# Kernel tuning notes

Hardware: AMD Instinct MI355X
Metric: run time of the kernel (lower is better)

## Reference

```python
import jax, jax.numpy as jnp
import numpy as np

B, D, H, W, Q = 16, 768, 64, 64, 128


def setup_inputs() -> dict:
    key = jax.random.key(0)
    ks = jax.random.split(key, 6)
    s = 0.02  # param init scale
    return {
        "visual_feat": jax.random.normal(ks[0], (B, D, H, W), jnp.float32),
        "text_feat": jax.random.normal(ks[1], (B, Q, D), jnp.float32),
        "Wq": jax.random.normal(ks[2], (D, D), jnp.float32) * s,
        "bq": jnp.zeros((D,), jnp.float32),
        "Wk": jax.random.normal(ks[3], (D, D), jnp.float32) * s,
        "bk": jnp.zeros((D,), jnp.float32),
        "Wv": jax.random.normal(ks[4], (D, D), jnp.float32) * s,
        "bv": jnp.zeros((D,), jnp.float32),
    }


def _entropy_weights(x):
    # x: [B, T, D] -> softmax over features, per-token entropy, softmax over tokens -> [B, T]
    p = jax.nn.softmax(x, axis=-1)
    ent = -jnp.sum(p * jnp.log(p + 1e-9), axis=-1)
    return jax.nn.softmax(ent, axis=-1)


def reference(visual_feat, text_feat, Wq, bq, Wk, bk, Wv, bv):
    b, d, h, w = visual_feat.shape
    vf = visual_feat.reshape(b, d, h * w).transpose(0, 2, 1)  # [B, N, D]
    ve = _entropy_weights(vf)          # [B, N]
    te = _entropy_weights(text_feat)   # [B, Q]
    q = vf @ Wq.T + bq                 # [B, N, D]
    k = text_feat @ Wk.T + bk          # [B, Q, D]
    v = text_feat @ Wv.T + bv          # [B, Q, D]
    attn = jnp.einsum('bnd,bqd->bnq', q, k) / jnp.sqrt(jnp.float32(d))
    attn = attn * (ve[:, :, None] * te[:, None, :])  # entropy outer-product modulation
    attn = jax.nn.softmax(attn, axis=-1)
    enhanced = jnp.einsum('bnq,bqd->bnd', attn, v)   # [B, N, D]
    return enhanced.transpose(0, 2, 1).reshape(b, d, h, w)
```

## Files before the change

kernel.cpp:

```cpp
#include <hip/hip_runtime.h>

#define B_ 16
#define D_ 768
#define N_ 4096
#define Q_ 128

typedef __attribute__((ext_vector_type(4))) float f32x4;
typedef __attribute__((ext_vector_type(8))) short short8;
typedef __attribute__((ext_vector_type(4))) short sv4;

__device__ __forceinline__ unsigned short f2bf(float f) {
  union { float f; unsigned u; } x; x.f = f;
  unsigned u = x.u;
  unsigned r = u + 0x7fffu + ((u >> 16) & 1u);
  return (unsigned short)(r >> 16);
}
__device__ __forceinline__ float bf2f(unsigned short h) {
  union { unsigned u; float f; } x; x.u = ((unsigned)h) << 16;
  return x.f;
}

__global__ __launch_bounds__(256) void prep_kernel(
    const float* __restrict__ Wk, const float* __restrict__ Wv,
    const float* __restrict__ Wq,
    unsigned short* __restrict__ Wkb, unsigned short* __restrict__ Wvb,
    unsigned short* __restrict__ WqTb) {
  __shared__ float tile[32][33];
  const int z = blockIdx.z;
  const int t = threadIdx.x;
  if (z <= 1) {
    const float* src = z ? Wv : Wk;
    unsigned short* dst = z ? Wvb : Wkb;
    int i = (blockIdx.y * 24 + blockIdx.x) * 256 + t;
    float4 v = ((const float4*)src)[i];
    ushort4 o;
    o.x = f2bf(v.x); o.y = f2bf(v.y); o.z = f2bf(v.z); o.w = f2bf(v.w);
    ((ushort4*)dst)[i] = o;
  } else {
    int bx = blockIdx.x * 32, by = blockIdx.y * 32;
    int tx = t & 31, ty = t >> 5;
    #pragma unroll
    for (int i = 0; i < 32; i += 8)
      tile[ty + i][tx] = Wq[(size_t)(by + ty + i) * D_ + bx + tx];
    __syncthreads();
    #pragma unroll
    for (int i = 0; i < 32; i += 8)
      WqTb[(size_t)(bx + ty + i) * D_ + by + tx] = f2bf(tile[tx][ty + i]);
  }
}

__global__ __launch_bounds__(256) void text_prep_kernel(
    const float* __restrict__ text, unsigned short* __restrict__ textb,
    float* __restrict__ ent_t) {
  int row = blockIdx.x * 4 + (threadIdx.x >> 6);
  int lane = threadIdx.x & 63;
  const float4* src = (const float4*)(text + (size_t)row * D_);
  ushort4* dst = (ushort4*)(textb + (size_t)row * D_);
  float s = 0.f, tt = 0.f;
  #pragma unroll
  for (int j = 0; j < 3; j++) {
    float4 v = src[lane + 64 * j];
    float e0 = __expf(v.x), e1 = __expf(v.y), e2 = __expf(v.z), e3 = __expf(v.w);
    s += (e0 + e1) + (e2 + e3);
    tt += v.x * e0 + v.y * e1;
    tt += v.z * e2 + v.w * e3;
    ushort4 o;
    o.x = f2bf(v.x); o.y = f2bf(v.y); o.z = f2bf(v.z); o.w = f2bf(v.w);
    dst[lane + 64 * j] = o;
  }
  #pragma unroll
  for (int off = 32; off; off >>= 1) {
    s += __shfl_xor(s, off);
    tt += __shfl_xor(tt, off);
  }
  if (lane == 0) ent_t[row] = __logf(s) - tt / s;
}

__global__ __launch_bounds__(1024) void softmax_fused_kernel(
    const float* __restrict__ ent_v, float* __restrict__ vew,
    const float* __restrict__ ent_t, float* __restrict__ tew) {
  __shared__ float red[32];
  __shared__ float sv[128];
  const int b = blockIdx.x, t = threadIdx.x;
  if (b < 16) {
    const float* e = ent_v + (size_t)b * N_;
    float v[4];
    float m = -__builtin_inff();
    #pragma unroll
    for (int i = 0; i < 4; i++) { v[i] = e[t + 1024 * i]; m = fmaxf(m, v[i]); }
    #pragma unroll
    for (int off = 32; off; off >>= 1) m = fmaxf(m, __shfl_xor(m, off));
    int wv = t >> 6;
    if ((t & 63) == 0) red[wv] = m;
    __syncthreads();
    if (t < 16) {
      float x = red[t];
      #pragma unroll
      for (int off = 8; off; off >>= 1) x = fmaxf(x, __shfl_xor(x, off));
      red[t] = x;
    }
    __syncthreads();
    m = red[0];
    float ev[4];
    float s = 0.f;
    #pragma unroll
    for (int i = 0; i < 4; i++) { ev[i] = __expf(v[i] - m); s += ev[i]; }
    #pragma unroll
    for (int off = 32; off; off >>= 1) s += __shfl_xor(s, off);
    __syncthreads();
    if ((t & 63) == 0) red[wv] = s;
    __syncthreads();
    if (t < 16) {
      float x = red[t];
      #pragma unroll
      for (int off = 8; off; off >>= 1) x += __shfl_xor(x, off);
      red[t] = x;
    }
    __syncthreads();
    s = red[0];
    #pragma unroll
    for (int i = 0; i < 4; i++) vew[(size_t)b * N_ + t + 1024 * i] = ev[i] / s;
  } else {
    const int bb = b - 16;
    float v = 0.f;
    if (t < 128) { v = ent_t[bb * 128 + t]; sv[t] = v; }
    __syncthreads();
    if (t < 64) {
      float m = fmaxf(sv[t], sv[t + 64]);
      #pragma unroll
      for (int off = 32; off; off >>= 1) m = fmaxf(m, __shfl_xor(m, off));
      if (t == 0) red[0] = m;
    }
    __syncthreads();
    const float m = red[0];
    float e = 0.f;
    if (t < 128) { e = __expf(v - m); sv[t] = e; }
    __syncthreads();
    if (t < 64) {
      float s = sv[t] + sv[t + 64];
      #pragma unroll
      for (int off = 32; off; off >>= 1) s += __shfl_xor(s, off);
      if (t == 0) red[1] = s;
    }
    __syncthreads();
    if (t < 128) tew[bb * 128 + t] = e / red[1];
  }
}

__global__ __launch_bounds__(256) void gemm_kvT_kernel(
    const unsigned short* __restrict__ A, const unsigned short* __restrict__ Wkb,
    const float* __restrict__ bk, unsigned short* __restrict__ kb,
    const unsigned short* __restrict__ Wvb, const float* __restrict__ bv,
    unsigned short* __restrict__ vTb) {
  constexpr int LDA = 72;
  __shared__ unsigned short As[64 * LDA];
  __shared__ unsigned short Bs[64 * LDA];
  const bool isV = blockIdx.y >= 12;
  const unsigned short* Bm = isV ? Wvb : Wkb;
  const float* bias = isV ? bv : bk;
  unsigned short* C = isV ? vTb : kb;
  int m0 = blockIdx.x * 64, n0 = (isV ? blockIdx.y - 12 : blockIdx.y) * 64;
  int t = threadIdx.x, wave = t >> 6, lane = t & 63;
  int wm = (wave & 1) * 32, wn = (wave >> 1) * 32;
  int fl = lane & 15, fq = lane >> 4;
  f32x4 acc[2][2];
  #pragma unroll
  for (int i = 0; i < 2; i++)
    #pragma unroll
    for (int j = 0; j < 2; j++) acc[i][j] = {0.f, 0.f, 0.f, 0.f};
  for (int k0 = 0; k0 < D_; k0 += 64) {
    __syncthreads();
    #pragma unroll
    for (int i = 0; i < 2; i++) {
      int c = t + 256 * i;
      int sr = c >> 3, sc = (c & 7) * 8;
      *(uint4*)(As + sr * LDA + sc) = *(const uint4*)(A + (size_t)(m0 + sr) * D_ + k0 + sc);
      *(uint4*)(Bs + sr * LDA + sc) = *(const uint4*)(Bm + (size_t)(n0 + sr) * D_ + k0 + sc);
    }
    __syncthreads();
    #pragma unroll
    for (int ks = 0; ks < 2; ks++) {
      short8 afr[2], bfr[2];
      #pragma unroll
      for (int i = 0; i < 2; i++)
        afr[i] = *(const short8*)(As + (wm + i * 16 + fl) * LDA + ks * 32 + fq * 8);
      #pragma unroll
      for (int j = 0; j < 2; j++)
        bfr[j] = *(const short8*)(Bs + (wn + j * 16 + fl) * LDA + ks * 32 + fq * 8);
      #pragma unroll
      for (int i = 0; i < 2; i++)
        #pragma unroll
        for (int j = 0; j < 2; j++)
          acc[i][j] = __builtin_amdgcn_mfma_f32_16x16x32_bf16(afr[i], bfr[j], acc[i][j], 0, 0, 0);
    }
  }
  #pragma unroll
  for (int i = 0; i < 2; i++)
    #pragma unroll
    for (int j = 0; j < 2; j++) {
      int n = n0 + wn + j * 16 + fl;
      float bb = bias[n];
      #pragma unroll
      for (int r = 0; r < 4; r++) {
        int m = m0 + wm + i * 16 + fq * 4 + r;
        float val = acc[i][j][r] + bb;
        if (isV) {
          int bt = m >> 7, q = m & 127;
          C[((size_t)bt * D_ + n) * Q_ + q] = f2bf(val);
        } else {
          C[(size_t)m * D_ + n] = f2bf(val);
        }
      }
    }
}

__global__ __launch_bounds__(256) void gemm_kq_bias_kernel(
    const unsigned short* __restrict__ kb, const unsigned short* __restrict__ WqTb,
    unsigned short* __restrict__ kqb, const float* __restrict__ bq,
    float* __restrict__ skq) {
  constexpr int LDA = 72;
  __shared__ unsigned short As[64 * LDA];
  __shared__ unsigned short Bs[64 * LDA];
  const int t = threadIdx.x;
  if (blockIdx.y >= 12) {
    int idx = (blockIdx.y - 12) * 32 + blockIdx.x;
    int row = idx * 4 + (t >> 6);
    int lane = t & 63;
    const unsigned short* kr = kb + (size_t)row * D_;
    float s = 0.f;
    for (int k = lane; k < D_; k += 64) s += bq[k] * bf2f(kr[k]);
    #pragma unroll
    for (int off = 32; off; off >>= 1) s += __shfl_xor(s, off);
    if (lane == 0) skq[row] = s;
    return;
  }
  int m0 = blockIdx.x * 64, n0 = blockIdx.y * 64;
  int wave = t >> 6, lane = t & 63;
  int wm = (wave & 1) * 32, wn = (wave >> 1) * 32;
  int fl = lane & 15, fq = lane >> 4;
  f32x4 acc[2][2];
  #pragma unroll
  for (int i = 0; i < 2; i++)
    #pragma unroll
    for (int j = 0; j < 2; j++) acc[i][j] = {0.f, 0.f, 0.f, 0.f};
  for (int k0 = 0; k0 < D_; k0 += 64) {
    __syncthreads();
    #pragma unroll
    for (int i = 0; i < 2; i++) {
      int c = t + 256 * i;
      int sr = c >> 3, sc = (c & 7) * 8;
      *(uint4*)(As + sr * LDA + sc) = *(const uint4*)(kb + (size_t)(m0 + sr) * D_ + k0 + sc);
      *(uint4*)(Bs + sr * LDA + sc) = *(const uint4*)(WqTb + (size_t)(n0 + sr) * D_ + k0 + sc);
    }
    __syncthreads();
    #pragma unroll
    for (int ks = 0; ks < 2; ks++) {
      short8 afr[2], bfr[2];
      #pragma unroll
      for (int i = 0; i < 2; i++)
        afr[i] = *(const short8*)(As + (wm + i * 16 + fl) * LDA + ks * 32 + fq * 8);
      #pragma unroll
      for (int j = 0; j < 2; j++)
        bfr[j] = *(const short8*)(Bs + (wn + j * 16 + fl) * LDA + ks * 32 + fq * 8);
      #pragma unroll
      for (int i = 0; i < 2; i++)
        #pragma unroll
        for (int j = 0; j < 2; j++)
          acc[i][j] = __builtin_amdgcn_mfma_f32_16x16x32_bf16(afr[i], bfr[j], acc[i][j], 0, 0, 0);
    }
  }
  #pragma unroll
  for (int i = 0; i < 2; i++)
    #pragma unroll
    for (int j = 0; j < 2; j++) {
      int n = n0 + wn + j * 16 + fl;
      #pragma unroll
      for (int r = 0; r < 4; r++) {
        int m = m0 + wm + i * 16 + fq * 4 + r;
        kqb[(size_t)m * D_ + n] = f2bf(acc[i][j][r]);
      }
    }
}

__global__ __launch_bounds__(256, 2) void attn_s_kernel(
    const float* __restrict__ vis,
    const unsigned short* __restrict__ kq,
    float* __restrict__ S,
    float* __restrict__ ent_v)
{
  constexpr int LA = 68;
  constexpr int LB = 72;
  __shared__ unsigned short As[64 * LA];
  __shared__ unsigned short Bs[128 * LB];
  __shared__ float esh[512];

  const int bb = blockIdx.x >> 6;
  const int n0 = (blockIdx.x & 63) * 64;
  const int t = threadIdx.x;
  const int wave = t >> 6, lane = t & 63;
  const int fl = lane & 15, fq = lane >> 4;
  const int wm = (wave & 1) * 32;
  const int wq = (wave >> 1) * 64;

  const float* abase = vis + (size_t)bb * D_ * N_ + n0;
  const unsigned short* bbase = kq + (size_t)bb * Q_ * D_;

  f32x4 acc[2][4];
  #pragma unroll
  for (int i = 0; i < 2; i++)
    #pragma unroll
    for (int j = 0; j < 4; j++) acc[i][j] = {0.f, 0.f, 0.f, 0.f};

  const int smi = t & 63;
  const int ph = t >> 6;
  float es = 0.f, ets = 0.f;

  for (int k0 = 0; k0 < D_; k0 += 64) {
    __syncthreads();
    #pragma unroll
    for (int i = 0; i < 8; i++) {
      const int kk = 2 * (ph + 4 * i);
      const float v0 = abase[(size_t)(k0 + kk) * N_ + smi];
      const float v1 = abase[(size_t)(k0 + kk + 1) * N_ + smi];
      const float e0 = __expf(v0), e1 = __expf(v1);
      es += e0 + e1;
      ets += v0 * e0 + v1 * e1;
      const unsigned pk = (unsigned)f2bf(v0) | ((unsigned)f2bf(v1) << 16);
      *(unsigned*)(As + smi * LA + kk) = pk;
    }
    #pragma unroll
    for (int i = 0; i < 4; i++) {
      const int c = t + 256 * i;
      const int q = c >> 3, kc = (c & 7) * 8;
      const uint4 v = *(const uint4*)(bbase + (size_t)q * D_ + k0 + kc);
      *(uint4*)(Bs + q * LB + kc) = v;
    }
    __syncthreads();
    #pragma unroll
    for (int ks = 0; ks < 2; ks++) {
      short8 afr[2], bfr[4];
      #pragma unroll
      for (int i = 0; i < 2; i++) {
        const unsigned short* pa = As + (wm + i * 16 + fl) * LA + ks * 32 + fq * 8;
        sv4 lo = *(const sv4*)pa;
        sv4 hi = *(const sv4*)(pa + 4);
        afr[i] = __builtin_shufflevector(lo, hi, 0, 1, 2, 3, 4, 5, 6, 7);
      }
      #pragma unroll
      for (int j = 0; j < 4; j++)
        bfr[j] = *(const short8*)(Bs + (wq + j * 16 + fl) * LB + ks * 32 + fq * 8);
      #pragma unroll
      for (int i = 0; i < 2; i++)
        #pragma unroll
        for (int j = 0; j < 4; j++)
          acc[i][j] = __builtin_amdgcn_mfma_f32_16x16x32_bf16(afr[i], bfr[j], acc[i][j], 0, 0, 0);
    }
  }

  esh[t] = es;
  esh[256 + t] = ets;
  __syncthreads();
  if (t < 64) {
    const float Sx = esh[t] + esh[t + 64] + esh[t + 128] + esh[t + 192];
    const float Tx = esh[256 + t] + esh[320 + t] + esh[384 + t] + esh[448 + t];
    ent_v[(size_t)bb * N_ + n0 + t] = __logf(Sx) - Tx / Sx;
  }

  float* sbase = S + ((size_t)bb * N_ + n0) * Q_;
  #pragma unroll
  for (int i = 0; i < 2; i++)
    #pragma unroll
    for (int j = 0; j < 4; j++)
      #pragma unroll
      for (int r = 0; r < 4; r++)
        sbase[(size_t)(wm + i * 16 + fq * 4 + r) * Q_ + wq + j * 16 + fl] = acc[i][j][r];
}

__global__ __launch_bounds__(256, 2) void attn_pv_kernel(
    const float* __restrict__ S,
    const unsigned short* __restrict__ vT,
    const float* __restrict__ ve,
    const float* __restrict__ te,
    const float* __restrict__ skq,
    float* __restrict__ out)
{
  constexpr int LP = 136;
  __shared__ unsigned short Ps[64 * LP];
  __shared__ unsigned short Vs[64 * LP];
  __shared__ float stats[2][64][2];

  const int bb = blockIdx.x >> 6;
  const int n0 = (blockIdx.x & 63) * 64;
  const int t = threadIdx.x;
  const int wave = t >> 6, lane = t & 63;
  const int fl = lane & 15, fq = lane >> 4;
  const int wm = (wave & 1) * 32;
  const int wq = (wave >> 1) * 64;

  f32x4 acc[2][4];
  const float* sbase = S + ((size_t)bb * N_ + n0) * Q_;
  #pragma unroll
  for (int i = 0; i < 2; i++)
    #pragma unroll
    for (int j = 0; j < 4; j++)
      #pragma unroll
      for (int r = 0; r < 4; r++)
        acc[i][j][r] = sbase[(size_t)(wm + i * 16 + fq * 4 + r) * Q_ + wq + j * 16 + fl];

  const float rsD = 0.03608439182435161f;
  float tev[4], skv[4];
  #pragma unroll
  for (int j = 0; j < 4; j++) {
    int q = wq + j * 16 + fl;
    tev[j] = te[bb * Q_ + q];
    skv[j] = skq[bb * Q_ + q];
  }
  float vev4[2][4];
  #pragma unroll
  for (int i = 0; i < 2; i++)
    #pragma unroll
    for (int r = 0; r < 4; r++)
      vev4[i][r] = ve[(size_t)bb * N_ + n0 + wm + i * 16 + fq * 4 + r];

  float rmax[2][4], rsum[2][4];
  #pragma unroll
  for (int i = 0; i < 2; i++)
    #pragma unroll
    for (int r = 0; r < 4; r++) rmax[i][r] = -__builtin_inff();
  #pragma unroll
  for (int i = 0; i < 2; i++)
    #pragma unroll
    for (int j = 0; j < 4; j++)
      #pragma unroll
      for (int r = 0; r < 4; r++) {
        float L = (acc[i][j][r] + skv[j]) * rsD * vev4[i][r] * tev[j];
        acc[i][j][r] = L;
        rmax[i][r] = fmaxf(rmax[i][r], L);
      }
  #pragma unroll
  for (int off = 1; off < 16; off <<= 1)
    #pragma unroll
    for (int i = 0; i < 2; i++)
      #pragma unroll
      for (int r = 0; r < 4; r++)
        rmax[i][r] = fmaxf(rmax[i][r], __shfl_xor(rmax[i][r], off));
  #pragma unroll
  for (int i = 0; i < 2; i++)
    #pragma unroll
    for (int r = 0; r < 4; r++) rsum[i][r] = 0.f;
  #pragma unroll
  for (int i = 0; i < 2; i++)
    #pragma unroll
    for (int j = 0; j < 4; j++)
      #pragma unroll
      for (int r = 0; r < 4; r++) {
        float e = __expf(acc[i][j][r] - rmax[i][r]);
        acc[i][j][r] = e;
        rsum[i][r] += e;
      }
  #pragma unroll
  for (int off = 1; off < 16; off <<= 1)
    #pragma unroll
    for (int i = 0; i < 2; i++)
      #pragma unroll
      for (int r = 0; r < 4; r++) rsum[i][r] += __shfl_xor(rsum[i][r], off);

  const int qh = wq >> 6;
  if (fl == 0) {
    #pragma unroll
    for (int i = 0; i < 2; i++)
      #pragma unroll
      for (int r = 0; r < 4; r++) {
        int m = wm + i * 16 + fq * 4 + r;
        stats[qh][m][0] = rmax[i][r];
        stats[qh][m][1] = rsum[i][r];
      }
  }
  __syncthreads();
  float fac[2][4];
  #pragma unroll
  for (int i = 0; i < 2; i++)
    #pragma unroll
    for (int r = 0; r < 4; r++) {
      int m = wm + i * 16 + fq * 4 + r;
      float M2 = stats[1 - qh][m][0], S2 = stats[1 - qh][m][1];
      float Mf = fmaxf(rmax[i][r], M2);
      float sf = rsum[i][r] * __expf(rmax[i][r] - Mf) + S2 * __expf(M2 - Mf);
      fac[i][r] = __expf(rmax[i][r] - Mf) / sf;
    }
  #pragma unroll
  for (int i = 0; i < 2; i++)
    #pragma unroll
    for (int j = 0; j < 4; j++)
      #pragma unroll
      for (int r = 0; r < 4; r++) {
        int m = wm + i * 16 + fq * 4 + r;
        int q = wq + j * 16 + fl;
        Ps[m * LP + q] = f2bf(acc[i][j][r] * fac[i][r]);
      }

  const int wd = (wave & 1) * 32;
  const int wm2 = (wave >> 1) * 32;
  for (int dc = 0; dc < 12; dc++) {
    __syncthreads();
    const unsigned short* vbase = vT + ((size_t)bb * D_ + dc * 64) * Q_;
    #pragma unroll
    for (int i = 0; i < 4; i++) {
      const int c = t + 256 * i;
      const int d = c >> 4, qc = (c & 15) * 8;
      *(uint4*)(Vs + d * LP + qc) = *(const uint4*)(vbase + (size_t)d * Q_ + qc);
    }
    __syncthreads();
    f32x4 acc2[2][2];
    #pragma unroll
    for (int i = 0; i < 2; i++)
      #pragma unroll
      for (int j = 0; j < 2; j++) acc2[i][j] = {0.f, 0.f, 0.f, 0.f};
    #pragma unroll
    for (int ks = 0; ks < 4; ks++) {
      short8 vfr[2], pfr[2];
      #pragma unroll
      for (int i = 0; i < 2; i++)
        vfr[i] = *(const short8*)(Vs + (wd + i * 16 + fl) * LP + ks * 32 + fq * 8);
      #pragma unroll
      for (int j = 0; j < 2; j++)
        pfr[j] = *(const short8*)(Ps + (wm2 + j * 16 + fl) * LP + ks * 32 + fq * 8);
      #pragma unroll
      for (int i = 0; i < 2; i++)
        #pragma unroll
        for (int j = 0; j < 2; j++)
          acc2[i][j] = __builtin_amdgcn_mfma_f32_16x16x32_bf16(vfr[i], pfr[j], acc2[i][j], 0, 0, 0);
    }
    float* obase = out + ((size_t)bb * D_ + dc * 64) * N_ + n0;
    #pragma unroll
    for (int i = 0; i < 2; i++)
      #pragma unroll
      for (int j = 0; j < 2; j++) {
        int mm = wm2 + j * 16 + fl;
        #pragma unroll
        for (int r = 0; r < 4; r++) {
          int d = wd + i * 16 + fq * 4 + r;
          obase[(size_t)d * N_ + mm] = acc2[i][j][r];
        }
      }
  }
}

extern "C" void kernel_launch(void* const* d_in, const int* in_sizes, int n_in,
                              void* d_out, int out_size, void* d_ws, size_t ws_size,
                              hipStream_t stream) {
  const float* vis  = (const float*)d_in[0];
  const float* text = (const float*)d_in[1];
  const float* Wq   = (const float*)d_in[2];
  const float* bq   = (const float*)d_in[3];
  const float* Wk   = (const float*)d_in[4];
  const float* bk   = (const float*)d_in[5];
  const float* Wv   = (const float*)d_in[6];
  const float* bv   = (const float*)d_in[7];
  float* out = (float*)d_out;
  char* ws = (char*)d_ws;

  unsigned short* textb = (unsigned short*)(ws + 0);
  unsigned short* Wkb   = (unsigned short*)(ws + 3145728);
  unsigned short* Wvb   = (unsigned short*)(ws + 4325376);
  unsigned short* WqTb  = (unsigned short*)(ws + 5505024);
  unsigned short* kb    = (unsigned short*)(ws + 6684672);
  unsigned short* kqb   = (unsigned short*)(ws + 9830400);
  unsigned short* vTb   = (unsigned short*)(ws + 12976128);
  float* ent_t = (float*)(ws + 16121856);
  float* tew   = (float*)(ws + 16130048);
  float* ent_v = (float*)(ws + 16138240);
  float* vew   = (float*)(ws + 16400384);
  float* skq   = (float*)(ws + 16662528);
  float* Sbuf  = (float*)(ws + 16777216);

  prep_kernel<<<dim3(24, 24, 3), 256, 0, stream>>>(Wk, Wv, Wq, Wkb, Wvb, WqTb);
  text_prep_kernel<<<512, 256, 0, stream>>>(text, textb, ent_t);
  gemm_kvT_kernel<<<dim3(32, 24), 256, 0, stream>>>(textb, Wkb, bk, kb, Wvb, bv, vTb);
  gemm_kq_bias_kernel<<<dim3(32, 28), 256, 0, stream>>>(kb, WqTb, kqb, bq, skq);
  attn_s_kernel<<<1024, 256, 0, stream>>>(vis, kqb, Sbuf, ent_v);
  softmax_fused_kernel<<<32, 1024, 0, stream>>>(ent_v, vew, ent_t, tew);
  attn_pv_kernel<<<1024, 256, 0, stream>>>(Sbuf, vTb, vew, tew, skq, out);
}
```

Baseline: 436.6 us.

## Fuse score, softmax and PV stages into one cooperative attention kernel

Adds a single attention kernel that computes the QK scores and the visual entropy. It then does a grid-wide sync so the per-batch entropy normaliser can be summed with atomics, applies the entropy modulation and softmax in registers, and multiplies by V. This avoids writing and re-reading the fp32 score buffer and drops two kernel launches. It needs all 1024 blocks to be co-resident through a cooperative launch, and falls back to the old three-kernel path if occupancy is too low or the launch fails. The Z accumulator is zeroed in the prep kernel.

```diff
diff --git a/kernel.cpp b/kernel.cpp
--- a/kernel.cpp
+++ b/kernel.cpp
@@ -1,4 +1,5 @@
 #include <hip/hip_runtime.h>
+#include <hip/hip_cooperative_groups.h>
 
 #define B_ 16
 #define D_ 768
@@ -24,7 +25,7 @@
     const float* __restrict__ Wk, const float* __restrict__ Wv,
     const float* __restrict__ Wq,
     unsigned short* __restrict__ Wkb, unsigned short* __restrict__ Wvb,
-    unsigned short* __restrict__ WqTb) {
+    unsigned short* __restrict__ WqTb, float* __restrict__ Zb) {
   __shared__ float tile[32][33];
   const int z = blockIdx.z;
   const int t = threadIdx.x;
@@ -46,6 +47,7 @@
     #pragma unroll
     for (int i = 0; i < 32; i += 8)
       WqTb[(size_t)(bx + ty + i) * D_ + by + tx] = f2bf(tile[tx][ty + i]);
+    if (blockIdx.x == 0 && blockIdx.y == 0 && t < 16) Zb[t] = 0.f;
   }
 }
 
@@ -282,6 +284,264 @@
     }
 }
 
+__global__ __launch_bounds__(256, 2) void attn_fused_kernel(
+    const float* __restrict__ vis,
+    const unsigned short* __restrict__ kq,
+    const unsigned short* __restrict__ vT,
+    const float* __restrict__ ent_t,
+    const float* __restrict__ skq,
+    float* __restrict__ Zb,
+    float* __restrict__ out)
+{
+  constexpr int LA = 68;
+  constexpr int LB = 72;
+  constexpr int LP = 136;
+  __shared__ unsigned short region0[17408];
+  __shared__ float stats[2][64][2];
+  __shared__ float tesh[128];
+  __shared__ float vesh[64];
+  __shared__ float zsh, tsum;
+  unsigned short* As = region0;
+  unsigned short* Bs = region0 + 4352;
+  float* esh = (float*)(region0 + 13568);
+  unsigned short* Ps = region0;
+  unsigned short* Vs = region0 + 8704;
+
+  const int bb = blockIdx.x >> 6;
+  const int n0 = (blockIdx.x & 63) * 64;
+  const int t = threadIdx.x;
+  const int wave = t >> 6, lane = t & 63;
+  const int fl = lane & 15, fq = lane >> 4;
+  const int wm = (wave & 1) * 32;
+  const int wq = (wave >> 1) * 64;
+
+  if (t < 128) tesh[t] = __expf(ent_t[bb * 128 + t]);
+  __syncthreads();
+  if (t < 64) {
+    float s = tesh[t] + tesh[t + 64];
+    #pragma unroll
+    for (int off = 32; off; off >>= 1) s += __shfl_xor(s, off);
+    if (t == 0) tsum = s;
+  }
+
+  const float* abase = vis + (size_t)bb * D_ * N_ + n0;
+  const unsigned short* bbase = kq + (size_t)bb * Q_ * D_;
+
+  f32x4 acc[2][4];
+  #pragma unroll
+  for (int i = 0; i < 2; i++)
+    #pragma unroll
+    for (int j = 0; j < 4; j++) acc[i][j] = {0.f, 0.f, 0.f, 0.f};
+
+  const int smi = t & 63;
+  const int ph = t >> 6;
+  float es = 0.f, ets = 0.f;
+
+  for (int k0 = 0; k0 < D_; k0 += 64) {
+    __syncthreads();
+    #pragma unroll
+    for (int i = 0; i < 8; i++) {
+      const int kk = 2 * (ph + 4 * i);
+      const float v0 = abase[(size_t)(k0 + kk) * N_ + smi];
+      const float v1 = abase[(size_t)(k0 + kk + 1) * N_ + smi];
+      const float e0 = __expf(v0), e1 = __expf(v1);
+      es += e0 + e1;
+      ets += v0 * e0 + v1 * e1;
+      const unsigned pk = (unsigned)f2bf(v0) | ((unsigned)f2bf(v1) << 16);
+      *(unsigned*)(As + smi * LA + kk) = pk;
+    }
+    #pragma unroll
+    for (int i = 0; i < 4; i++) {
+      const int c = t + 256 * i;
+      const int q = c >> 3, kc = (c & 7) * 8;
+      const uint4 v = *(const uint4*)(bbase + (size_t)q * D_ + k0 + kc);
+      *(uint4*)(Bs + q * LB + kc) = v;
+    }
+    __syncthreads();
+    #pragma unroll
+    for (int ks = 0; ks < 2; ks++) {
+      short8 afr[2], bfr[4];
+      #pragma unroll
+      for (int i = 0; i < 2; i++) {
+        const unsigned short* pa = As + (wm + i * 16 + fl) * LA + ks * 32 + fq * 8;
+        sv4 lo = *(const sv4*)pa;
+        sv4 hi = *(const sv4*)(pa + 4);
+        afr[i] = __builtin_shufflevector(lo, hi, 0, 1, 2, 3, 4, 5, 6, 7);
+      }
+      #pragma unroll
+      for (int j = 0; j < 4; j++)
+        bfr[j] = *(const short8*)(Bs + (wq + j * 16 + fl) * LB + ks * 32 + fq * 8);
+      #pragma unroll
+      for (int i = 0; i < 2; i++)
+        #pragma unroll
+        for (int j = 0; j < 4; j++)
+          acc[i][j] = __builtin_amdgcn_mfma_f32_16x16x32_bf16(afr[i], bfr[j], acc[i][j], 0, 0, 0);
+    }
+  }
+
+  __syncthreads();
+  esh[t] = es;
+  esh[256 + t] = ets;
+  __syncthreads();
+  if (t < 64) {
+    const float Sx = esh[t] + esh[t + 64] + esh[t + 128] + esh[t + 192];
+    const float Tx = esh[256 + t] + esh[320 + t] + esh[384 + t] + esh[448 + t];
+    const float ent = __logf(Sx) - Tx / Sx;
+    const float ev = __expf(ent);
+    vesh[t] = ev;
+    float s = ev;
+    #pragma unroll
+    for (int off = 32; off; off >>= 1) s += __shfl_xor(s, off);
+    if (t == 0) {
+      atomicAdd(&Zb[bb], s);
+      __threadfence();
+    }
+  }
+  cooperative_groups::this_grid().sync();
+  if (t == 0) zsh = atomicAdd(&Zb[bb], 0.0f);
+  __syncthreads();
+  const float rZ = 1.0f / zsh;
+  const float rT = 1.0f / tsum;
+
+  const float rsD = 0.03608439182435161f;
+  float tev[4], skv[4];
+  #pragma unroll
+  for (int j = 0; j < 4; j++) {
+    int q = wq + j * 16 + fl;
+    tev[j] = tesh[q] * rT;
+    skv[j] = skq[bb * Q_ + q];
+  }
+  float vev4[2][4];
+  #pragma unroll
+  for (int i = 0; i < 2; i++)
+    #pragma unroll
+    for (int r = 0; r < 4; r++)
+      vev4[i][r] = vesh[wm + i * 16 + fq * 4 + r] * rZ;
+
+  float rmax[2][4], rsum[2][4];
+  #pragma unroll
+  for (int i = 0; i < 2; i++)
+    #pragma unroll
+    for (int r = 0; r < 4; r++) rmax[i][r] = -__builtin_inff();
+  #pragma unroll
+  for (int i = 0; i < 2; i++)
+    #pragma unroll
+    for (int j = 0; j < 4; j++)
+      #pragma unroll
+      for (int r = 0; r < 4; r++) {
+        float L = (acc[i][j][r] + skv[j]) * rsD * vev4[i][r] * tev[j];
+        acc[i][j][r] = L;
+        rmax[i][r] = fmaxf(rmax[i][r], L);
+      }
+  #pragma unroll
+  for (int off = 1; off < 16; off <<= 1)
+    #pragma unroll
+    for (int i = 0; i < 2; i++)
+      #pragma unroll
+      for (int r = 0; r < 4; r++)
+        rmax[i][r] = fmaxf(rmax[i][r], __shfl_xor(rmax[i][r], off));
+  #pragma unroll
+  for (int i = 0; i < 2; i++)
+    #pragma unroll
+    for (int r = 0; r < 4; r++) rsum[i][r] = 0.f;
+  #pragma unroll
+  for (int i = 0; i < 2; i++)
+    #pragma unroll
+    for (int j = 0; j < 4; j++)
+      #pragma unroll
+      for (int r = 0; r < 4; r++) {
+        float e = __expf(acc[i][j][r] - rmax[i][r]);
+        acc[i][j][r] = e;
+        rsum[i][r] += e;
+      }
+  #pragma unroll
+  for (int off = 1; off < 16; off <<= 1)
+    #pragma unroll
+    for (int i = 0; i < 2; i++)
+      #pragma unroll
+      for (int r = 0; r < 4; r++) rsum[i][r] += __shfl_xor(rsum[i][r], off);
+
+  const int qh = wq >> 6;
+  if (fl == 0) {
+    #pragma unroll
+    for (int i = 0; i < 2; i++)
+      #pragma unroll
+      for (int r = 0; r < 4; r++) {
+        int m = wm + i * 16 + fq * 4 + r;
+        stats[qh][m][0] = rmax[i][r];
+        stats[qh][m][1] = rsum[i][r];
+      }
+  }
+  __syncthreads();
+  float fac[2][4];
+  #pragma unroll
+  for (int i = 0; i < 2; i++)
+    #pragma unroll
+    for (int r = 0; r < 4; r++) {
+      int m = wm + i * 16 + fq * 4 + r;
+      float M2 = stats[1 - qh][m][0], S2 = stats[1 - qh][m][1];
+      float Mf = fmaxf(rmax[i][r], M2);
+      float sf = rsum[i][r] * __expf(rmax[i][r] - Mf) + S2 * __expf(M2 - Mf);
+      fac[i][r] = __expf(rmax[i][r] - Mf) / sf;
+    }
+  #pragma unroll
+  for (int i = 0; i < 2; i++)
+    #pragma unroll
+    for (int j = 0; j < 4; j++)
+      #pragma unroll
+      for (int r = 0; r < 4; r++) {
+        int m = wm + i * 16 + fq * 4 + r;
+        int q = wq + j * 16 + fl;
+        Ps[m * LP + q] = f2bf(acc[i][j][r] * fac[i][r]);
+      }
+
+  const int wd = (wave & 1) * 32;
+  const int wm2 = (wave >> 1) * 32;
+  for (int dc = 0; dc < 12; dc++) {
+    __syncthreads();
+    const unsigned short* vbase = vT + ((size_t)bb * D_ + dc * 64) * Q_;
+    #pragma unroll
+    for (int i = 0; i < 4; i++) {
+      const int c = t + 256 * i;
+      const int d = c >> 4, qc = (c & 15) * 8;
+      *(uint4*)(Vs + d * LP + qc) = *(const uint4*)(vbase + (size_t)d * Q_ + qc);
+    }
+    __syncthreads();
+    f32x4 acc2[2][2];
+    #pragma unroll
+    for (int i = 0; i < 2; i++)
+      #pragma unroll
+      for (int j = 0; j < 2; j++) acc2[i][j] = {0.f, 0.f, 0.f, 0.f};
+    #pragma unroll
+    for (int ks = 0; ks < 4; ks++) {
+      short8 vfr[2], pfr[2];
+      #pragma unroll
+      for (int i = 0; i < 2; i++)
+        vfr[i] = *(const short8*)(Vs + (wd + i * 16 + fl) * LP + ks * 32 + fq * 8);
+      #pragma unroll
+      for (int j = 0; j < 2; j++)
+        pfr[j] = *(const short8*)(Ps + (wm2 + j * 16 + fl) * LP + ks * 32 + fq * 8);
+      #pragma unroll
+      for (int i = 0; i < 2; i++)
+        #pragma unroll
+        for (int j = 0; j < 2; j++)
+          acc2[i][j] = __builtin_amdgcn_mfma_f32_16x16x32_bf16(vfr[i], pfr[j], acc2[i][j], 0, 0, 0);
+    }
+    float* obase = out + ((size_t)bb * D_ + dc * 64) * N_ + n0;
+    #pragma unroll
+    for (int i = 0; i < 2; i++)
+      #pragma unroll
+      for (int j = 0; j < 2; j++) {
+        int mm = wm2 + j * 16 + fl;
+        #pragma unroll
+        for (int r = 0; r < 4; r++) {
+          int d = wd + i * 16 + fq * 4 + r;
+          obase[(size_t)d * N_ + mm] = acc2[i][j][r];
+        }
+      }
+  }
+}
+
 __global__ __launch_bounds__(256, 2) void attn_s_kernel(
     const float* __restrict__ vis,
     const unsigned short* __restrict__ kq,
@@ -572,13 +832,28 @@
   float* ent_v = (float*)(ws + 16138240);
   float* vew   = (float*)(ws + 16400384);
   float* skq   = (float*)(ws + 16662528);
+  float* Zb    = (float*)(ws + 16664576);
   float* Sbuf  = (float*)(ws + 16777216);
 
-  prep_kernel<<<dim3(24, 24, 3), 256, 0, stream>>>(Wk, Wv, Wq, Wkb, Wvb, WqTb);
+  prep_kernel<<<dim3(24, 24, 3), 256, 0, stream>>>(Wk, Wv, Wq, Wkb, Wvb, WqTb, Zb);
   text_prep_kernel<<<512, 256, 0, stream>>>(text, textb, ent_t);
   gemm_kvT_kernel<<<dim3(32, 24), 256, 0, stream>>>(textb, Wkb, bk, kb, Wvb, bv, vTb);
   gemm_kq_bias_kernel<<<dim3(32, 28), 256, 0, stream>>>(kb, WqTb, kqb, bq, skq);
-  attn_s_kernel<<<1024, 256, 0, stream>>>(vis, kqb, Sbuf, ent_v);
-  softmax_fused_kernel<<<32, 1024, 0, stream>>>(ent_v, vew, ent_t, tew);
-  attn_pv_kernel<<<1024, 256, 0, stream>>>(Sbuf, vTb, vew, tew, skq, out);
-}
+
+  int blocksPerCU = 0;
+  hipOccupancyMaxActiveBlocksPerMultiprocessor(&blocksPerCU,
+      (const void*)attn_fused_kernel, 256, 0);
+  bool coop = blocksPerCU >= 4;
+  if (coop) {
+    void* args[] = {(void*)&vis, (void*)&kqb, (void*)&vTb, (void*)&ent_t,
+                    (void*)&skq, (void*)&Zb, (void*)&out};
+    hipError_t ce = hipLaunchCooperativeKernel((const void*)attn_fused_kernel,
+                                               dim3(1024), dim3(256), args, 0, stream);
+    if (ce != hipSuccess) { coop = false; (void)hipGetLastError(); }
+  }
+  if (!coop) {
+    attn_s_kernel<<<1024, 256, 0, stream>>>(vis, kqb, Sbuf, ent_v);
+    softmax_fused_kernel<<<32, 1024, 0, stream>>>(ent_v, vew, ent_t, tew);
+    attn_pv_kernel<<<1024, 256, 0, stream>>>(Sbuf, vTb, vew, tew, skq, out);
+  }
+}
```

Measured after the change: 435.9 us. No clear change (-0.2%).

## Fuse text prep into weight prep and entropy softmax into attn_pv

Applied to the files above, without the earlier changes.

The text bf16 conversion and entropy computation move into an extra z-slice of the weight prep kernel. The separate softmax kernel is removed: each attn_pv block now recomputes the per-batch normaliser over 4096 visual entropies and the 128 text entropies, then exponentiates them locally. This drops two launches and their global round-trips. In exchange every block redundantly reads 4096 entropy values, and the max subtraction is gone, which is only safe while entropies stay small (they are bounded by log 768).

```diff
diff --git a/kernel.cpp b/kernel.cpp
--- a/kernel.cpp
+++ b/kernel.cpp
@@ -22,9 +22,10 @@
 
 __global__ __launch_bounds__(256) void prep_kernel(
     const float* __restrict__ Wk, const float* __restrict__ Wv,
-    const float* __restrict__ Wq,
+    const float* __restrict__ Wq, const float* __restrict__ text,
     unsigned short* __restrict__ Wkb, unsigned short* __restrict__ Wvb,
-    unsigned short* __restrict__ WqTb) {
+    unsigned short* __restrict__ WqTb, unsigned short* __restrict__ textb,
+    float* __restrict__ ent_t) {
   __shared__ float tile[32][33];
   const int z = blockIdx.z;
   const int t = threadIdx.x;
@@ -36,7 +37,7 @@
     ushort4 o;
     o.x = f2bf(v.x); o.y = f2bf(v.y); o.z = f2bf(v.z); o.w = f2bf(v.w);
     ((ushort4*)dst)[i] = o;
-  } else {
+  } else if (z == 2) {
     int bx = blockIdx.x * 32, by = blockIdx.y * 32;
     int tx = t & 31, ty = t >> 5;
     #pragma unroll
@@ -46,104 +47,31 @@
     #pragma unroll
     for (int i = 0; i < 32; i += 8)
       WqTb[(size_t)(bx + ty + i) * D_ + by + tx] = f2bf(tile[tx][ty + i]);
-  }
-}
-
-__global__ __launch_bounds__(256) void text_prep_kernel(
-    const float* __restrict__ text, unsigned short* __restrict__ textb,
-    float* __restrict__ ent_t) {
-  int row = blockIdx.x * 4 + (threadIdx.x >> 6);
-  int lane = threadIdx.x & 63;
-  const float4* src = (const float4*)(text + (size_t)row * D_);
-  ushort4* dst = (ushort4*)(textb + (size_t)row * D_);
-  float s = 0.f, tt = 0.f;
-  #pragma unroll
-  for (int j = 0; j < 3; j++) {
-    float4 v = src[lane + 64 * j];
-    float e0 = __expf(v.x), e1 = __expf(v.y), e2 = __expf(v.z), e3 = __expf(v.w);
-    s += (e0 + e1) + (e2 + e3);
-    tt += v.x * e0 + v.y * e1;
-    tt += v.z * e2 + v.w * e3;
-    ushort4 o;
-    o.x = f2bf(v.x); o.y = f2bf(v.y); o.z = f2bf(v.z); o.w = f2bf(v.w);
-    dst[lane + 64 * j] = o;
-  }
-  #pragma unroll
-  for (int off = 32; off; off >>= 1) {
-    s += __shfl_xor(s, off);
-    tt += __shfl_xor(tt, off);
-  }
-  if (lane == 0) ent_t[row] = __logf(s) - tt / s;
-}
-
-__global__ __launch_bounds__(1024) void softmax_fused_kernel(
-    const float* __restrict__ ent_v, float* __restrict__ vew,
-    const float* __restrict__ ent_t, float* __restrict__ tew) {
-  __shared__ float red[32];
-  __shared__ float sv[128];
-  const int b = blockIdx.x, t = threadIdx.x;
-  if (b < 16) {
-    const float* e = ent_v + (size_t)b * N_;
-    float v[4];
-    float m = -__builtin_inff();
-    #pragma unroll
-    for (int i = 0; i < 4; i++) { v[i] = e[t + 1024 * i]; m = fmaxf(m, v[i]); }
-    #pragma unroll
-    for (int off = 32; off; off >>= 1) m = fmaxf(m, __shfl_xor(m, off));
-    int wv = t >> 6;
-    if ((t & 63) == 0) red[wv] = m;
-    __syncthreads();
-    if (t < 16) {
-      float x = red[t];
-      #pragma unroll
-      for (int off = 8; off; off >>= 1) x = fmaxf(x, __shfl_xor(x, off));
-      red[t] = x;
-    }
-    __syncthreads();
-    m = red[0];
-    float ev[4];
-    float s = 0.f;
-    #pragma unroll
-    for (int i = 0; i < 4; i++) { ev[i] = __expf(v[i] - m); s += ev[i]; }
-    #pragma unroll
-    for (int off = 32; off; off >>= 1) s += __shfl_xor(s, off);
-    __syncthreads();
-    if ((t & 63) == 0) red[wv] = s;
-    __syncthreads();
-    if (t < 16) {
-      float x = red[t];
-      #pragma unroll
-      for (int off = 8; off; off >>= 1) x += __shfl_xor(x, off);
-      red[t] = x;
-    }
-    __syncthreads();
-    s = red[0];
-    #pragma unroll
-    for (int i = 0; i < 4; i++) vew[(size_t)b * N_ + t + 1024 * i] = ev[i] / s;
   } else {
-    const int bb = b - 16;
-    float v = 0.f;
-    if (t < 128) { v = ent_t[bb * 128 + t]; sv[t] = v; }
-    __syncthreads();
-    if (t < 64) {
-      float m = fmaxf(sv[t], sv[t + 64]);
-      #pragma unroll
-      for (int off = 32; off; off >>= 1) m = fmaxf(m, __shfl_xor(m, off));
-      if (t == 0) red[0] = m;
-    }
-    __syncthreads();
-    const float m = red[0];
-    float e = 0.f;
-    if (t < 128) { e = __expf(v - m); sv[t] = e; }
-    __syncthreads();
-    if (t < 64) {
-      float s = sv[t] + sv[t + 64];
-      #pragma unroll
-      for (int off = 32; off; off >>= 1) s += __shfl_xor(s, off);
-      if (t == 0) red[1] = s;
-    }
-    __syncthreads();
-    if (t < 128) tew[bb * 128 + t] = e / red[1];
+    int idx = blockIdx.y * 24 + blockIdx.x;
+    if (idx >= 512) return;
+    int row = idx * 4 + (t >> 6);
+    int lane = t & 63;
+    const float4* src = (const float4*)(text + (size_t)row * D_);
+    ushort4* dst = (ushort4*)(textb + (size_t)row * D_);
+    float s = 0.f, tt = 0.f;
+    #pragma unroll
+    for (int j = 0; j < 3; j++) {
+      float4 v = src[lane + 64 * j];
+      float e0 = __expf(v.x), e1 = __expf(v.y), e2 = __expf(v.z), e3 = __expf(v.w);
+      s += (e0 + e1) + (e2 + e3);
+      tt += v.x * e0 + v.y * e1;
+      tt += v.z * e2 + v.w * e3;
+      ushort4 o;
+      o.x = f2bf(v.x); o.y = f2bf(v.y); o.z = f2bf(v.z); o.w = f2bf(v.w);
+      dst[lane + 64 * j] = o;
+    }
+    #pragma unroll
+    for (int off = 32; off; off >>= 1) {
+      s += __shfl_xor(s, off);
+      tt += __shfl_xor(tt, off);
+    }
+    if (lane == 0) ent_t[row] = __logf(s) - tt / s;
   }
 }
 
@@ -379,8 +307,8 @@
 __global__ __launch_bounds__(256, 2) void attn_pv_kernel(
     const float* __restrict__ S,
     const unsigned short* __restrict__ vT,
-    const float* __restrict__ ve,
-    const float* __restrict__ te,
+    const float* __restrict__ ent_v,
+    const float* __restrict__ ent_t,
     const float* __restrict__ skq,
     float* __restrict__ out)
 {
@@ -388,6 +316,10 @@
   __shared__ unsigned short Ps[64 * LP];
   __shared__ unsigned short Vs[64 * LP];
   __shared__ float stats[2][64][2];
+  __shared__ float tesh[128];
+  __shared__ float vesh[64];
+  __shared__ float zred[4];
+  __shared__ float zsum, tsum;
 
   const int bb = blockIdx.x >> 6;
   const int n0 = (blockIdx.x & 63) * 64;
@@ -397,6 +329,27 @@
   const int wm = (wave & 1) * 32;
   const int wq = (wave >> 1) * 64;
 
+  const float* evb = ent_v + (size_t)bb * N_;
+  float zp = 0.f;
+  #pragma unroll
+  for (int i = 0; i < 16; i++) zp += __expf(evb[t + 256 * i]);
+  #pragma unroll
+  for (int off = 32; off; off >>= 1) zp += __shfl_xor(zp, off);
+  if (lane == 0) zred[wave] = zp;
+  if (t < 128) tesh[t] = __expf(ent_t[bb * 128 + t]);
+  if (t < 64) vesh[t] = __expf(evb[n0 + t]);
+  __syncthreads();
+  if (t == 0) zsum = zred[0] + zred[1] + zred[2] + zred[3];
+  if (t < 64) {
+    float s = tesh[t] + tesh[t + 64];
+    #pragma unroll
+    for (int off = 32; off; off >>= 1) s += __shfl_xor(s, off);
+    if (t == 0) tsum = s;
+  }
+  __syncthreads();
+  const float rZ = 1.0f / zsum;
+  const float rT = 1.0f / tsum;
+
   f32x4 acc[2][4];
   const float* sbase = S + ((size_t)bb * N_ + n0) * Q_;
   #pragma unroll
@@ -412,7 +365,7 @@
   #pragma unroll
   for (int j = 0; j < 4; j++) {
     int q = wq + j * 16 + fl;
-    tev[j] = te[bb * Q_ + q];
+    tev[j] = tesh[q] * rT;
     skv[j] = skq[bb * Q_ + q];
   }
   float vev4[2][4];
@@ -420,7 +373,7 @@
   for (int i = 0; i < 2; i++)
     #pragma unroll
     for (int r = 0; r < 4; r++)
-      vev4[i][r] = ve[(size_t)bb * N_ + n0 + wm + i * 16 + fq * 4 + r];
+      vev4[i][r] = vesh[wm + i * 16 + fq * 4 + r] * rZ;
 
   float rmax[2][4], rsum[2][4];
   #pragma unroll
@@ -568,17 +521,14 @@
   unsigned short* kqb   = (unsigned short*)(ws + 9830400);
   unsigned short* vTb   = (unsigned short*)(ws + 12976128);
   float* ent_t = (float*)(ws + 16121856);
-  float* tew   = (float*)(ws + 16130048);
   float* ent_v = (float*)(ws + 16138240);
-  float* vew   = (float*)(ws + 16400384);
   float* skq   = (float*)(ws + 16662528);
   float* Sbuf  = (float*)(ws + 16777216);
 
-  prep_kernel<<<dim3(24, 24, 3), 256, 0, stream>>>(Wk, Wv, Wq, Wkb, Wvb, WqTb);
-  text_prep_kernel<<<512, 256, 0, stream>>>(text, textb, ent_t);
+  prep_kernel<<<dim3(24, 24, 4), 256, 0, stream>>>(Wk, Wv, Wq, text,
+                                                   Wkb, Wvb, WqTb, textb, ent_t);
   gemm_kvT_kernel<<<dim3(32, 24), 256, 0, stream>>>(textb, Wkb, bk, kb, Wvb, bv, vTb);
   gemm_kq_bias_kernel<<<dim3(32, 28), 256, 0, stream>>>(kb, WqTb, kqb, bq, skq);
   attn_s_kernel<<<1024, 256, 0, stream>>>(vis, kqb, Sbuf, ent_v);
-  softmax_fused_kernel<<<32, 1024, 0, stream>>>(ent_v, vew, ent_t, tew);
-  attn_pv_kernel<<<1024, 256, 0, stream>>>(Sbuf, vTb, vew, tew, skq, out);
-}
+  attn_pv_kernel<<<1024, 256, 0, stream>>>(Sbuf, vTb, ent_v, ent_t, skq, out);
+}
```

New measurement: 430.7 us. No clear change (-1.4%).
